# Optimization experiments

Measured on AMD Instinct MI355X. Metric: run time of the kernel, lower is better.

## Reference

```python
import jax, jax.numpy as jnp
import numpy as np

T, B, D_IN, D_HID, D_OUT = 2048, 64, 256, 256, 256


def setup_inputs() -> dict:
    key = jax.random.key(0)
    k1, k2, k3, k4 = jax.random.split(key, 4)
    s_in = 1.0 / np.sqrt(D_IN)
    s_h = 1.0 / np.sqrt(D_HID)
    return {
        "x": jax.random.normal(k1, (T, B, D_IN), dtype=jnp.float32),
        "h": jnp.zeros((B, D_HID), dtype=jnp.float32),
        "W_in": jax.random.uniform(k2, (D_HID, D_IN), jnp.float32, -s_in, s_in),
        "W_hid": jax.random.uniform(k3, (D_HID, D_HID), jnp.float32, -s_h, s_h),
        "W_out": jax.random.uniform(k4, (D_OUT, D_HID), jnp.float32, -s_h, s_h),
    }


def reference(x, h, W_in, W_hid, W_out):
    # Precompute input projections for all timesteps in one big matmul: [T,B,H]
    x_proj = jnp.einsum("tbi,hi->tbh", x, W_in)

    def step(h_prev, xp_t):
        h_new = jnp.tanh(xp_t + h_prev @ W_hid.T)
        return h_new, h_new

    h_last, hs = jax.lax.scan(step, h, x_proj)  # hs: [T,B,H]
    ys = jnp.einsum("tbh,oh->tbo", hs, W_out).reshape(-1, W_out.shape[0])
    return ys, h_last
```

## Files before the change

kernel.cpp:

```cpp
#include <hip/hip_runtime.h>
#include <hip/hip_bf16.h>

#define TSTEPS 2048
#define NB 64
#define DH 256
#define NBDH (NB * DH)

typedef __attribute__((ext_vector_type(8))) short short8;
typedef __attribute__((ext_vector_type(4))) float f32x4;
typedef __attribute__((ext_vector_type(4))) int i32x4;

#define WSCALE 2032.0f
#define HSCALE 127.0f
#define INVSC (1.0f / (2032.0f * 127.0f))

__device__ __forceinline__ unsigned short f2bf(float f) {
  union { float f; unsigned u; } v; v.f = f;
  unsigned u = v.u;
  u += 0x7FFFu + ((u >> 16) & 1u);
  return (unsigned short)(u >> 16);
}

__device__ __forceinline__ float fast_tanh(float x) {
  float e = __builtin_amdgcn_exp2f(x * 2.885390081777927f);
  return 1.0f - 2.0f * __builtin_amdgcn_rcpf(e + 1.0f);
}

__device__ __forceinline__ int p2c(int p) {
  int q = p & 31;
  return (p & ~31) | ((q & 1) << 4) | (q >> 1);
}

__global__ void cvt_w(const float* __restrict__ win, const float* __restrict__ whid,
                      const float* __restrict__ wout, unsigned short* __restrict__ wbf,
                      char* __restrict__ wq) {
  int i = blockIdx.x * 256 + threadIdx.x;
  int mat = i >> 16, idx = i & 65535;
  int n = idx >> 8, klin = idx & 255;
  if (mat == 0) {
    wbf[idx] = f2bf(win[idx]);
  } else {
    const float* m = (mat == 1) ? whid : wout;
    float v = m[n * 256 + p2c(klin)] * WSCALE;
    int q = (int)__builtin_rintf(fminf(fmaxf(v, -127.f), 127.f));
    wq[(mat - 1) * 65536 + idx] = (char)q;
  }
}

__global__ __launch_bounds__(256) void gemm_in(
    const float* __restrict__ x, const unsigned short* __restrict__ Wbf,
    float* __restrict__ Cout) {
  const int w = threadIdx.x >> 6, l = threadIdx.x & 63;
  const int m16 = l & 15, kg = l >> 4;
  const long tile0 = ((long)blockIdx.x * 4 + w) * 2;

  short8 afr[2][8];
  for (int ti = 0; ti < 2; ++ti) {
    const float* ar = x + ((tile0 + ti) * 16 + m16) * 256 + kg * 8;
    for (int ks = 0; ks < 8; ++ks) {
      float4 f0 = *(const float4*)(ar + ks * 32);
      float4 f1 = *(const float4*)(ar + ks * 32 + 4);
      short8 s;
      s[0] = (short)f2bf(f0.x); s[1] = (short)f2bf(f0.y);
      s[2] = (short)f2bf(f0.z); s[3] = (short)f2bf(f0.w);
      s[4] = (short)f2bf(f1.x); s[5] = (short)f2bf(f1.y);
      s[6] = (short)f2bf(f1.z); s[7] = (short)f2bf(f1.w);
      afr[ti][ks] = s;
    }
  }
  for (int nt = 0; nt < 16; ++nt) {
    const int n = nt * 16 + m16;
    const unsigned short* wr = Wbf + n * 256 + kg * 8;
    f32x4 acc0 = {0.f, 0.f, 0.f, 0.f}, acc1 = {0.f, 0.f, 0.f, 0.f};
    for (int ks = 0; ks < 8; ++ks) {
      short8 b = *(const short8*)(wr + ks * 32);
      acc0 = __builtin_amdgcn_mfma_f32_16x16x32_bf16(afr[0][ks], b, acc0, 0, 0, 0);
      acc1 = __builtin_amdgcn_mfma_f32_16x16x32_bf16(afr[1][ks], b, acc1, 0, 0, 0);
    }
    for (int r = 0; r < 4; ++r) {
      Cout[(tile0 * 16 + kg * 4 + r) * 256 + n]       = acc0[r];
      Cout[((tile0 + 1) * 16 + kg * 4 + r) * 256 + n] = acc1[r];
    }
  }
}

__global__ __launch_bounds__(512, 2) void rnn_scan(
    const float* __restrict__ xp, const char* __restrict__ Wq,
    const float* __restrict__ h0, float* __restrict__ ys,
    float* __restrict__ hlast) {
  __shared__ __align__(16) char hq[2][256];
  const int tid = threadIdx.x, w = tid >> 6, l = tid & 63;
  const int b = blockIdx.x;
  const int m16 = l & 15, kg = l >> 4;

  i32x4 bq[2][4], by[2][4];
  for (int nt = 0; nt < 2; ++nt) {
    const char* wr = Wq + (w * 32 + nt * 16 + m16) * 256 + kg * 16;
    for (int ks = 0; ks < 4; ++ks) {
      bq[nt][ks] = *(const i32x4*)(wr + ks * 64);
      by[nt][ks] = *(const i32x4*)(wr + 65536 + ks * 64);
    }
  }

  if (tid < 256) {
    float v = fminf(fmaxf(h0[b * 256 + p2c(tid)], -1.f), 1.f) * HSCALE;
    hq[0][tid] = (char)(int)__builtin_rintf(v);
  }
  __syncthreads();

  const char* rda = &hq[0][0] + kg * 16;
  const float* xpb = xp + (long)b * 256 + w * 32 + m16;
  float* ysb = ys + (long)b * 256 + w * 32 + l;

  float xv0[2], xv1[2], xv2[2], xv3[2];
  if (l < 16) {
    xv0[0] = xpb[0];               xv0[1] = xpb[16];
    xv1[0] = xpb[1L * NBDH];       xv1[1] = xpb[1L * NBDH + 16];
    xv2[0] = xpb[2L * NBDH];       xv2[1] = xpb[2L * NBDH + 16];
    xv3[0] = xpb[3L * NBDH];       xv3[1] = xpb[3L * NBDH + 16];
  }

#define MI8(A, B, C) __builtin_amdgcn_mfma_i32_16x16x64_i8(A, B, C, 0, 0, 0)
#define RNN_STEP(T, CUR, XV, PF)                                              \
  {                                                                           \
    const char* ap = rda + (CUR) * 256;                                       \
    i32x4 a0 = *(const i32x4*)(ap);                                           \
    i32x4 a1 = *(const i32x4*)(ap + 64);                                      \
    i32x4 a2 = *(const i32x4*)(ap + 128);                                     \
    i32x4 a3 = *(const i32x4*)(ap + 192);                                     \
    float xq0 = XV[0], xq1 = XV[1];         \
    i32x4 c0 = {0, 0, 0, 0}, c1 = {0, 0, 0, 0};                               \
    if ((PF) && l < 16) {               \
      const float* q = xpb + (long)((T) + 4) * NBDH;                          \
      XV[0] = q[0]; XV[1] = q[16];                                            \
    }                                                                         \
    c0 = MI8(a0, bq[0][0], c0); c1 = MI8(a0, bq[1][0], c1);                   \
    c0 = MI8(a1, bq[0][1], c0); c1 = MI8(a1, bq[1][1], c1);                   \
    c0 = MI8(a2, bq[0][2], c0); c1 = MI8(a2, bq[1][2], c1);                   \
    c0 = MI8(a3, bq[0][3], c0); c1 = MI8(a3, bq[1][3], c1);                   \
    i32x4 y0 = {0, 0, 0, 0}, y1 = {0, 0, 0, 0};   \
    y0 = MI8(a0, by[0][0], y0); y1 = MI8(a0, by[1][0], y1);                   \
    y0 = MI8(a1, by[0][1], y0); y1 = MI8(a1, by[1][1], y1);                   \
    y0 = MI8(a2, by[0][2], y0); y1 = MI8(a2, by[1][2], y1);                   \
    y0 = MI8(a3, by[0][3], y0); y1 = MI8(a3, by[1][3], y1);                   \
    float z0 = (float)c0[0] * INVSC + xq0;                                    \
    float z1 = (float)c1[0] * INVSC + xq1;                                    \
    float t0 = fast_tanh(z0), t1 = fast_tanh(z1);                             \
    int q0 = (int)__builtin_rintf(t0 * HSCALE);                               \
    int q1 = (int)__builtin_rintf(t1 * HSCALE);                               \
    unsigned short uq = (unsigned short)((q0 & 0xFF) | ((q1 & 0xFF) << 8));   \
    if (l < 16) {                                                             \
      *(unsigned short*)(&hq[(CUR) ^ 1][w * 32 + 2 * l]) = uq;                \
      if ((T) > 0) {                                                          \
        ysb[(long)((T) - 1) * NBDH]      = (float)y0[0] * INVSC;              \
        ysb[(long)((T) - 1) * NBDH + 16] = (float)y1[0] * INVSC;              \
      }                                                                       \
      if ((T) == TSTEPS - 1) {                                                \
        hlast[b * 256 + w * 32 + l]      = t0;                                \
        hlast[b * 256 + w * 32 + 16 + l] = t1;                                \
      }                                                                       \
    }                                                                         \
    asm volatile("s_waitcnt lgkmcnt(0)" ::: "memory");    \
    __builtin_amdgcn_s_barrier();                                             \
    __builtin_amdgcn_sched_barrier(0);                                        \
  }

#pragma unroll 1
  for (int t = 0; t < TSTEPS - 4; t += 4) {
    RNN_STEP(t, 0, xv0, true);
    RNN_STEP(t + 1, 1, xv1, true);
    RNN_STEP(t + 2, 0, xv2, true);
    RNN_STEP(t + 3, 1, xv3, true);
  }
  RNN_STEP(TSTEPS - 4, 0, xv0, false);
  RNN_STEP(TSTEPS - 3, 1, xv1, false);
  RNN_STEP(TSTEPS - 2, 0, xv2, false);
  RNN_STEP(TSTEPS - 1, 1, xv3, false);
#undef RNN_STEP

  {
    const char* ap = rda;
    i32x4 a0 = *(const i32x4*)(ap);
    i32x4 a1 = *(const i32x4*)(ap + 64);
    i32x4 a2 = *(const i32x4*)(ap + 128);
    i32x4 a3 = *(const i32x4*)(ap + 192);
    i32x4 y0 = {0, 0, 0, 0}, y1 = {0, 0, 0, 0};
    y0 = MI8(a0, by[0][0], y0); y1 = MI8(a0, by[1][0], y1);
    y0 = MI8(a1, by[0][1], y0); y1 = MI8(a1, by[1][1], y1);
    y0 = MI8(a2, by[0][2], y0); y1 = MI8(a2, by[1][2], y1);
    y0 = MI8(a3, by[0][3], y0); y1 = MI8(a3, by[1][3], y1);
    if (l < 16) {
      ysb[(long)(TSTEPS - 1) * NBDH]      = (float)y0[0] * INVSC;
      ysb[(long)(TSTEPS - 1) * NBDH + 16] = (float)y1[0] * INVSC;
    }
  }
#undef MI8
}

extern "C" void kernel_launch(void* const* d_in, const int* in_sizes, int n_in,
                              void* d_out, int out_size, void* d_ws, size_t ws_size,
                              hipStream_t stream) {
  const float* x    = (const float*)d_in[0];
  const float* h0   = (const float*)d_in[1];
  const float* Win  = (const float*)d_in[2];
  const float* Whid = (const float*)d_in[3];
  const float* Wout = (const float*)d_in[4];
  float* ys    = (float*)d_out;
  float* hlast = ys + (long)TSTEPS * NB * 256;

  unsigned short* wbf_in = (unsigned short*)d_ws;
  char* wq = (char*)d_ws + 131072;
  float* xproj = (float*)((char*)d_ws + 262144);

  cvt_w<<<dim3(768), dim3(256), 0, stream>>>(Win, Whid, Wout, wbf_in, wq);
  gemm_in<<<dim3(1024), dim3(256), 0, stream>>>(x, wbf_in, xproj);
  rnn_scan<<<dim3(64), dim3(512), 0, stream>>>(xproj, wq, h0, ys, hlast);
}
```

Before: 954.9 us.

## Split recurrence and output projection across separate waves; store input projection as packed bf16

```diff
diff --git a/kernel.cpp b/kernel.cpp
--- a/kernel.cpp
+++ b/kernel.cpp
@@ -49,7 +49,7 @@
 
 __global__ __launch_bounds__(256) void gemm_in(
     const float* __restrict__ x, const unsigned short* __restrict__ Wbf,
-    float* __restrict__ Cout) {
+    unsigned* __restrict__ xpk) {
   const int w = threadIdx.x >> 6, l = threadIdx.x & 63;
   const int m16 = l & 15, kg = l >> 4;
   const long tile0 = ((long)blockIdx.x * 4 + w) * 2;
@@ -68,37 +68,50 @@
       afr[ti][ks] = s;
     }
   }
-  for (int nt = 0; nt < 16; ++nt) {
-    const int n = nt * 16 + m16;
-    const unsigned short* wr = Wbf + n * 256 + kg * 8;
-    f32x4 acc0 = {0.f, 0.f, 0.f, 0.f}, acc1 = {0.f, 0.f, 0.f, 0.f};
+  for (int g = 0; g < 8; ++g) {
+    const unsigned short* wr0 = Wbf + (g * 32 + m16) * 256 + kg * 8;
+    const unsigned short* wr1 = Wbf + (g * 32 + 16 + m16) * 256 + kg * 8;
+    f32x4 a00 = {0,0,0,0}, a01 = {0,0,0,0}, a10 = {0,0,0,0}, a11 = {0,0,0,0};
     for (int ks = 0; ks < 8; ++ks) {
-      short8 b = *(const short8*)(wr + ks * 32);
-      acc0 = __builtin_amdgcn_mfma_f32_16x16x32_bf16(afr[0][ks], b, acc0, 0, 0, 0);
-      acc1 = __builtin_amdgcn_mfma_f32_16x16x32_bf16(afr[1][ks], b, acc1, 0, 0, 0);
+      short8 b0 = *(const short8*)(wr0 + ks * 32);
+      short8 b1 = *(const short8*)(wr1 + ks * 32);
+      a00 = __builtin_amdgcn_mfma_f32_16x16x32_bf16(afr[0][ks], b0, a00, 0, 0, 0);
+      a10 = __builtin_amdgcn_mfma_f32_16x16x32_bf16(afr[1][ks], b0, a10, 0, 0, 0);
+      a01 = __builtin_amdgcn_mfma_f32_16x16x32_bf16(afr[0][ks], b1, a01, 0, 0, 0);
+      a11 = __builtin_amdgcn_mfma_f32_16x16x32_bf16(afr[1][ks], b1, a11, 0, 0, 0);
     }
     for (int r = 0; r < 4; ++r) {
-      Cout[(tile0 * 16 + kg * 4 + r) * 256 + n]       = acc0[r];
-      Cout[((tile0 + 1) * 16 + kg * 4 + r) * 256 + n] = acc1[r];
-    }
-  }
-}
-
-__global__ __launch_bounds__(512, 2) void rnn_scan(
-    const float* __restrict__ xp, const char* __restrict__ Wq,
+      unsigned p0, p1;
+      asm("v_cvt_pk_bf16_f32 %0, %1, %2" : "=v"(p0) : "v"(a00[r]), "v"(a01[r]));
+      asm("v_cvt_pk_bf16_f32 %0, %1, %2" : "=v"(p1) : "v"(a10[r]), "v"(a11[r]));
+      xpk[(tile0 * 16 + kg * 4 + r) * 128 + g * 16 + m16]       = p0;
+      xpk[((tile0 + 1) * 16 + kg * 4 + r) * 128 + g * 16 + m16] = p1;
+    }
+  }
+}
+
+__global__ __launch_bounds__(768, 1) void rnn_scan(
+    const unsigned* __restrict__ xpk, const char* __restrict__ Wq,
     const float* __restrict__ h0, float* __restrict__ ys,
     float* __restrict__ hlast) {
   __shared__ __align__(16) char hq[2][256];
-  const int tid = threadIdx.x, w = tid >> 6, l = tid & 63;
+  const int tid = threadIdx.x, wid = tid >> 6, l = tid & 63;
   const int b = blockIdx.x;
   const int m16 = l & 15, kg = l >> 4;
-
-  i32x4 bq[2][4], by[2][4];
-  for (int nt = 0; nt < 2; ++nt) {
-    const char* wr = Wq + (w * 32 + nt * 16 + m16) * 256 + kg * 16;
-    for (int ks = 0; ks < 4; ++ks) {
-      bq[nt][ks] = *(const i32x4*)(wr + ks * 64);
-      by[nt][ks] = *(const i32x4*)(wr + 65536 + ks * 64);
+  const bool isy = (wid >= 8);
+  const int w = isy ? (wid - 8) : wid;
+
+  i32x4 bq[2][4];
+  i32x4 by[4][4];
+  if (!isy) {
+    for (int nt = 0; nt < 2; ++nt) {
+      const char* wr = Wq + (w * 32 + nt * 16 + m16) * 256 + kg * 16;
+      for (int ks = 0; ks < 4; ++ks) bq[nt][ks] = *(const i32x4*)(wr + ks * 64);
+    }
+  } else {
+    for (int nt = 0; nt < 4; ++nt) {
+      const char* wr = Wq + 65536 + (w * 64 + nt * 16 + m16) * 256 + kg * 16;
+      for (int ks = 0; ks < 4; ++ks) by[nt][ks] = *(const i32x4*)(wr + ks * 64);
     }
   }
 
@@ -109,15 +122,15 @@
   __syncthreads();
 
   const char* rda = &hq[0][0] + kg * 16;
-  const float* xpb = xp + (long)b * 256 + w * 32 + m16;
-  float* ysb = ys + (long)b * 256 + w * 32 + l;
-
-  float xv0[2], xv1[2], xv2[2], xv3[2];
-  if (l < 16) {
-    xv0[0] = xpb[0];               xv0[1] = xpb[16];
-    xv1[0] = xpb[1L * NBDH];       xv1[1] = xpb[1L * NBDH + 16];
-    xv2[0] = xpb[2L * NBDH];       xv2[1] = xpb[2L * NBDH + 16];
-    xv3[0] = xpb[3L * NBDH];       xv3[1] = xpb[3L * NBDH + 16];
+  const unsigned* xpb = xpk + (long)b * 128 + w * 16 + l;
+  float* ysb = ys + (long)b * 256 + w * 64 + l;
+
+  unsigned xv0 = 0, xv1 = 0, xv2 = 0, xv3 = 0;
+  if (!isy && l < 16) {
+    xv0 = xpb[0];
+    xv1 = xpb[1L * 8192];
+    xv2 = xpb[2L * 8192];
+    xv3 = xpb[3L * 8192];
   }
 
 #define MI8(A, B, C) __builtin_amdgcn_mfma_i32_16x16x64_i8(A, B, C, 0, 0, 0)
@@ -128,36 +141,45 @@
     i32x4 a1 = *(const i32x4*)(ap + 64);                                      \
     i32x4 a2 = *(const i32x4*)(ap + 128);                                     \
     i32x4 a3 = *(const i32x4*)(ap + 192);                                     \
-    float xq0 = XV[0], xq1 = XV[1];         \
-    i32x4 c0 = {0, 0, 0, 0}, c1 = {0, 0, 0, 0};                               \
-    if ((PF) && l < 16) {               \
-      const float* q = xpb + (long)((T) + 4) * NBDH;                          \
-      XV[0] = q[0]; XV[1] = q[16];                                            \
-    }                                                                         \
-    c0 = MI8(a0, bq[0][0], c0); c1 = MI8(a0, bq[1][0], c1);                   \
-    c0 = MI8(a1, bq[0][1], c0); c1 = MI8(a1, bq[1][1], c1);                   \
-    c0 = MI8(a2, bq[0][2], c0); c1 = MI8(a2, bq[1][2], c1);                   \
-    c0 = MI8(a3, bq[0][3], c0); c1 = MI8(a3, bq[1][3], c1);                   \
-    i32x4 y0 = {0, 0, 0, 0}, y1 = {0, 0, 0, 0};   \
-    y0 = MI8(a0, by[0][0], y0); y1 = MI8(a0, by[1][0], y1);                   \
-    y0 = MI8(a1, by[0][1], y0); y1 = MI8(a1, by[1][1], y1);                   \
-    y0 = MI8(a2, by[0][2], y0); y1 = MI8(a2, by[1][2], y1);                   \
-    y0 = MI8(a3, by[0][3], y0); y1 = MI8(a3, by[1][3], y1);                   \
-    float z0 = (float)c0[0] * INVSC + xq0;                                    \
-    float z1 = (float)c1[0] * INVSC + xq1;                                    \
-    float t0 = fast_tanh(z0), t1 = fast_tanh(z1);                             \
-    int q0 = (int)__builtin_rintf(t0 * HSCALE);                               \
-    int q1 = (int)__builtin_rintf(t1 * HSCALE);                               \
-    unsigned short uq = (unsigned short)((q0 & 0xFF) | ((q1 & 0xFF) << 8));   \
-    if (l < 16) {                                                             \
-      *(unsigned short*)(&hq[(CUR) ^ 1][w * 32 + 2 * l]) = uq;                \
-      if ((T) > 0) {                                                          \
-        ysb[(long)((T) - 1) * NBDH]      = (float)y0[0] * INVSC;              \
-        ysb[(long)((T) - 1) * NBDH + 16] = (float)y1[0] * INVSC;              \
+    if (!isy) {                                                               \
+      unsigned xc = XV;                     \
+      if ((PF) && l < 16) XV = xpb[(long)((T) + 4) * 8192];                   \
+      i32x4 c0 = {0, 0, 0, 0}, c1 = {0, 0, 0, 0};                             \
+      c0 = MI8(a0, bq[0][0], c0); c1 = MI8(a0, bq[1][0], c1);                 \
+      c0 = MI8(a1, bq[0][1], c0); c1 = MI8(a1, bq[1][1], c1);                 \
+      c0 = MI8(a2, bq[0][2], c0); c1 = MI8(a2, bq[1][2], c1);                 \
+      c0 = MI8(a3, bq[0][3], c0); c1 = MI8(a3, bq[1][3], c1);                 \
+      union { unsigned u; float f; } u0, u1;                                  \
+      u0.u = xc << 16; u1.u = xc & 0xffff0000u;                               \
+      float z0 = (float)c0[0] * INVSC + u0.f;                                 \
+      float z1 = (float)c1[0] * INVSC + u1.f;                                 \
+      float t0 = fast_tanh(z0), t1 = fast_tanh(z1);                           \
+      int q0 = (int)__builtin_rintf(t0 * HSCALE);                             \
+      int q1 = (int)__builtin_rintf(t1 * HSCALE);                             \
+      unsigned short uq = (unsigned short)((q0 & 0xFF) | ((q1 & 0xFF) << 8)); \
+      if (l < 16) {                                                           \
+        *(unsigned short*)(&hq[(CUR) ^ 1][w * 32 + 2 * l]) = uq;              \
+        if ((T) == TSTEPS - 1) {                                              \
+          hlast[b * 256 + w * 32 + l]      = t0;                              \
+          hlast[b * 256 + w * 32 + 16 + l] = t1;                              \
+        }                                                                     \
       }                                                                       \
-      if ((T) == TSTEPS - 1) {                                                \
-        hlast[b * 256 + w * 32 + l]      = t0;                                \
-        hlast[b * 256 + w * 32 + 16 + l] = t1;                                \
+    } else {                                                                  \
+      i32x4 y0 = {0,0,0,0}, y1 = {0,0,0,0}, y2 = {0,0,0,0}, y3 = {0,0,0,0};   \
+      y0 = MI8(a0, by[0][0], y0); y1 = MI8(a0, by[1][0], y1);                 \
+      y2 = MI8(a0, by[2][0], y2); y3 = MI8(a0, by[3][0], y3);                 \
+      y0 = MI8(a1, by[0][1], y0); y1 = MI8(a1, by[1][1], y1);                 \
+      y2 = MI8(a1, by[2][1], y2); y3 = MI8(a1, by[3][1], y3);                 \
+      y0 = MI8(a2, by[0][2], y0); y1 = MI8(a2, by[1][2], y1);                 \
+      y2 = MI8(a2, by[2][2], y2); y3 = MI8(a2, by[3][2], y3);                 \
+      y0 = MI8(a3, by[0][3], y0); y1 = MI8(a3, by[1][3], y1);                 \
+      y2 = MI8(a3, by[2][3], y2); y3 = MI8(a3, by[3][3], y3);                 \
+      if ((T) > 0 && l < 16) {                    \
+        float* yr = ysb + (long)((T) - 1) * NBDH;                             \
+        yr[0]  = (float)y0[0] * INVSC;                                        \
+        yr[16] = (float)y1[0] * INVSC;                                        \
+        yr[32] = (float)y2[0] * INVSC;                                        \
+        yr[48] = (float)y3[0] * INVSC;                                        \
       }                                                                       \
     }                                                                         \
     asm volatile("s_waitcnt lgkmcnt(0)" ::: "memory");    \
@@ -178,20 +200,27 @@
   RNN_STEP(TSTEPS - 1, 1, xv3, false);
 #undef RNN_STEP
 
-  {
+  if (isy) {
     const char* ap = rda;
     i32x4 a0 = *(const i32x4*)(ap);
     i32x4 a1 = *(const i32x4*)(ap + 64);
     i32x4 a2 = *(const i32x4*)(ap + 128);
     i32x4 a3 = *(const i32x4*)(ap + 192);
-    i32x4 y0 = {0, 0, 0, 0}, y1 = {0, 0, 0, 0};
+    i32x4 y0 = {0,0,0,0}, y1 = {0,0,0,0}, y2 = {0,0,0,0}, y3 = {0,0,0,0};
     y0 = MI8(a0, by[0][0], y0); y1 = MI8(a0, by[1][0], y1);
+    y2 = MI8(a0, by[2][0], y2); y3 = MI8(a0, by[3][0], y3);
     y0 = MI8(a1, by[0][1], y0); y1 = MI8(a1, by[1][1], y1);
+    y2 = MI8(a1, by[2][1], y2); y3 = MI8(a1, by[3][1], y3);
     y0 = MI8(a2, by[0][2], y0); y1 = MI8(a2, by[1][2], y1);
+    y2 = MI8(a2, by[2][2], y2); y3 = MI8(a2, by[3][2], y3);
     y0 = MI8(a3, by[0][3], y0); y1 = MI8(a3, by[1][3], y1);
+    y2 = MI8(a3, by[2][3], y2); y3 = MI8(a3, by[3][3], y3);
     if (l < 16) {
-      ysb[(long)(TSTEPS - 1) * NBDH]      = (float)y0[0] * INVSC;
-      ysb[(long)(TSTEPS - 1) * NBDH + 16] = (float)y1[0] * INVSC;
+      float* yr = ysb + (long)(TSTEPS - 1) * NBDH;
+      yr[0]  = (float)y0[0] * INVSC;
+      yr[16] = (float)y1[0] * INVSC;
+      yr[32] = (float)y2[0] * INVSC;
+      yr[48] = (float)y3[0] * INVSC;
     }
   }
 #undef MI8
@@ -210,9 +239,9 @@
 
   unsigned short* wbf_in = (unsigned short*)d_ws;
   char* wq = (char*)d_ws + 131072;
-  float* xproj = (float*)((char*)d_ws + 262144);
+  unsigned* xpk = (unsigned*)((char*)d_ws + 262144);
 
   cvt_w<<<dim3(768), dim3(256), 0, stream>>>(Win, Whid, Wout, wbf_in, wq);
-  gemm_in<<<dim3(1024), dim3(256), 0, stream>>>(x, wbf_in, xproj);
-  rnn_scan<<<dim3(64), dim3(512), 0, stream>>>(xproj, wq, h0, ys, hlast);
-}
+  gemm_in<<<dim3(1024), dim3(256), 0, stream>>>(x, wbf_in, xpk);
+  rnn_scan<<<dim3(64), dim3(768), 0, stream>>>(xpk, wq, h0, ys, hlast);
+}
```

New measurement: 1.010 ms. 1.06x slower.

## Move output projection out of serial scan into separate int8 GEMM; store xproj as bf16

Applied to the files above, without the earlier changes.

```diff
diff --git a/kernel.cpp b/kernel.cpp
--- a/kernel.cpp
+++ b/kernel.cpp
@@ -49,7 +49,7 @@
 
 __global__ __launch_bounds__(256) void gemm_in(
     const float* __restrict__ x, const unsigned short* __restrict__ Wbf,
-    float* __restrict__ Cout) {
+    unsigned* __restrict__ xpk) {
   const int w = threadIdx.x >> 6, l = threadIdx.x & 63;
   const int m16 = l & 15, kg = l >> 4;
   const long tile0 = ((long)blockIdx.x * 4 + w) * 2;
@@ -68,38 +68,41 @@
       afr[ti][ks] = s;
     }
   }
-  for (int nt = 0; nt < 16; ++nt) {
-    const int n = nt * 16 + m16;
-    const unsigned short* wr = Wbf + n * 256 + kg * 8;
-    f32x4 acc0 = {0.f, 0.f, 0.f, 0.f}, acc1 = {0.f, 0.f, 0.f, 0.f};
+  for (int g = 0; g < 8; ++g) {
+    const unsigned short* wr0 = Wbf + (g * 32 + m16) * 256 + kg * 8;
+    const unsigned short* wr1 = Wbf + (g * 32 + 16 + m16) * 256 + kg * 8;
+    f32x4 a00 = {0,0,0,0}, a01 = {0,0,0,0}, a10 = {0,0,0,0}, a11 = {0,0,0,0};
     for (int ks = 0; ks < 8; ++ks) {
-      short8 b = *(const short8*)(wr + ks * 32);
-      acc0 = __builtin_amdgcn_mfma_f32_16x16x32_bf16(afr[0][ks], b, acc0, 0, 0, 0);
-      acc1 = __builtin_amdgcn_mfma_f32_16x16x32_bf16(afr[1][ks], b, acc1, 0, 0, 0);
+      short8 b0 = *(const short8*)(wr0 + ks * 32);
+      short8 b1 = *(const short8*)(wr1 + ks * 32);
+      a00 = __builtin_amdgcn_mfma_f32_16x16x32_bf16(afr[0][ks], b0, a00, 0, 0, 0);
+      a10 = __builtin_amdgcn_mfma_f32_16x16x32_bf16(afr[1][ks], b0, a10, 0, 0, 0);
+      a01 = __builtin_amdgcn_mfma_f32_16x16x32_bf16(afr[0][ks], b1, a01, 0, 0, 0);
+      a11 = __builtin_amdgcn_mfma_f32_16x16x32_bf16(afr[1][ks], b1, a11, 0, 0, 0);
     }
     for (int r = 0; r < 4; ++r) {
-      Cout[(tile0 * 16 + kg * 4 + r) * 256 + n]       = acc0[r];
-      Cout[((tile0 + 1) * 16 + kg * 4 + r) * 256 + n] = acc1[r];
+      unsigned p0, p1;
+      asm("v_cvt_pk_bf16_f32 %0, %1, %2" : "=v"(p0) : "v"(a00[r]), "v"(a01[r]));
+      asm("v_cvt_pk_bf16_f32 %0, %1, %2" : "=v"(p1) : "v"(a10[r]), "v"(a11[r]));
+      xpk[(tile0 * 16 + kg * 4 + r) * 128 + g * 16 + m16]       = p0;
+      xpk[((tile0 + 1) * 16 + kg * 4 + r) * 128 + g * 16 + m16] = p1;
     }
   }
 }
 
 __global__ __launch_bounds__(512, 2) void rnn_scan(
-    const float* __restrict__ xp, const char* __restrict__ Wq,
-    const float* __restrict__ h0, float* __restrict__ ys,
+    const unsigned* __restrict__ xpk, const char* __restrict__ Wq,
+    const float* __restrict__ h0, char* __restrict__ hsq,
     float* __restrict__ hlast) {
   __shared__ __align__(16) char hq[2][256];
   const int tid = threadIdx.x, w = tid >> 6, l = tid & 63;
   const int b = blockIdx.x;
   const int m16 = l & 15, kg = l >> 4;
 
-  i32x4 bq[2][4], by[2][4];
+  i32x4 bq[2][4];
   for (int nt = 0; nt < 2; ++nt) {
     const char* wr = Wq + (w * 32 + nt * 16 + m16) * 256 + kg * 16;
-    for (int ks = 0; ks < 4; ++ks) {
-      bq[nt][ks] = *(const i32x4*)(wr + ks * 64);
-      by[nt][ks] = *(const i32x4*)(wr + 65536 + ks * 64);
-    }
+    for (int ks = 0; ks < 4; ++ks) bq[nt][ks] = *(const i32x4*)(wr + ks * 64);
   }
 
   if (tid < 256) {
@@ -109,15 +112,15 @@
   __syncthreads();
 
   const char* rda = &hq[0][0] + kg * 16;
-  const float* xpb = xp + (long)b * 256 + w * 32 + m16;
-  float* ysb = ys + (long)b * 256 + w * 32 + l;
-
-  float xv0[2], xv1[2], xv2[2], xv3[2];
+  const unsigned* xpb = xpk + (long)b * 128 + w * 16 + l;
+  char* hsb = hsq + (long)b * 256 + w * 32 + 2 * m16;
+
+  unsigned xv0 = 0, xv1 = 0, xv2 = 0, xv3 = 0;
   if (l < 16) {
-    xv0[0] = xpb[0];               xv0[1] = xpb[16];
-    xv1[0] = xpb[1L * NBDH];       xv1[1] = xpb[1L * NBDH + 16];
-    xv2[0] = xpb[2L * NBDH];       xv2[1] = xpb[2L * NBDH + 16];
-    xv3[0] = xpb[3L * NBDH];       xv3[1] = xpb[3L * NBDH + 16];
+    xv0 = xpb[0];
+    xv1 = xpb[1L * 8192];
+    xv2 = xpb[2L * 8192];
+    xv3 = xpb[3L * 8192];
   }
 
 #define MI8(A, B, C) __builtin_amdgcn_mfma_i32_16x16x64_i8(A, B, C, 0, 0, 0)
@@ -128,33 +131,24 @@
     i32x4 a1 = *(const i32x4*)(ap + 64);                                      \
     i32x4 a2 = *(const i32x4*)(ap + 128);                                     \
     i32x4 a3 = *(const i32x4*)(ap + 192);                                     \
-    float xq0 = XV[0], xq1 = XV[1];         \
+    unsigned xc = XV;                       \
     i32x4 c0 = {0, 0, 0, 0}, c1 = {0, 0, 0, 0};                               \
-    if ((PF) && l < 16) {               \
-      const float* q = xpb + (long)((T) + 4) * NBDH;                          \
-      XV[0] = q[0]; XV[1] = q[16];                                            \
-    }                                                                         \
+    if ((PF) && l < 16) XV = xpb[(long)((T) + 4) * 8192];                     \
     c0 = MI8(a0, bq[0][0], c0); c1 = MI8(a0, bq[1][0], c1);                   \
     c0 = MI8(a1, bq[0][1], c0); c1 = MI8(a1, bq[1][1], c1);                   \
     c0 = MI8(a2, bq[0][2], c0); c1 = MI8(a2, bq[1][2], c1);                   \
     c0 = MI8(a3, bq[0][3], c0); c1 = MI8(a3, bq[1][3], c1);                   \
-    i32x4 y0 = {0, 0, 0, 0}, y1 = {0, 0, 0, 0};   \
-    y0 = MI8(a0, by[0][0], y0); y1 = MI8(a0, by[1][0], y1);                   \
-    y0 = MI8(a1, by[0][1], y0); y1 = MI8(a1, by[1][1], y1);                   \
-    y0 = MI8(a2, by[0][2], y0); y1 = MI8(a2, by[1][2], y1);                   \
-    y0 = MI8(a3, by[0][3], y0); y1 = MI8(a3, by[1][3], y1);                   \
-    float z0 = (float)c0[0] * INVSC + xq0;                                    \
-    float z1 = (float)c1[0] * INVSC + xq1;                                    \
+    union { unsigned u; float f; } u0, u1;                                    \
+    u0.u = xc << 16; u1.u = xc & 0xffff0000u;                                 \
+    float z0 = (float)c0[0] * INVSC + u0.f;                                   \
+    float z1 = (float)c1[0] * INVSC + u1.f;                                   \
     float t0 = fast_tanh(z0), t1 = fast_tanh(z1);                             \
     int q0 = (int)__builtin_rintf(t0 * HSCALE);                               \
     int q1 = (int)__builtin_rintf(t1 * HSCALE);                               \
     unsigned short uq = (unsigned short)((q0 & 0xFF) | ((q1 & 0xFF) << 8));   \
     if (l < 16) {                                                             \
       *(unsigned short*)(&hq[(CUR) ^ 1][w * 32 + 2 * l]) = uq;                \
-      if ((T) > 0) {                                                          \
-        ysb[(long)((T) - 1) * NBDH]      = (float)y0[0] * INVSC;              \
-        ysb[(long)((T) - 1) * NBDH + 16] = (float)y1[0] * INVSC;              \
-      }                                                                       \
+      *(unsigned short*)(hsb + (long)(T) * NBDH) = uq;                        \
       if ((T) == TSTEPS - 1) {                                                \
         hlast[b * 256 + w * 32 + l]      = t0;                                \
         hlast[b * 256 + w * 32 + 16 + l] = t1;                                \
@@ -177,24 +171,35 @@
   RNN_STEP(TSTEPS - 2, 0, xv2, false);
   RNN_STEP(TSTEPS - 1, 1, xv3, false);
 #undef RNN_STEP
-
-  {
-    const char* ap = rda;
-    i32x4 a0 = *(const i32x4*)(ap);
-    i32x4 a1 = *(const i32x4*)(ap + 64);
-    i32x4 a2 = *(const i32x4*)(ap + 128);
-    i32x4 a3 = *(const i32x4*)(ap + 192);
-    i32x4 y0 = {0, 0, 0, 0}, y1 = {0, 0, 0, 0};
-    y0 = MI8(a0, by[0][0], y0); y1 = MI8(a0, by[1][0], y1);
-    y0 = MI8(a1, by[0][1], y0); y1 = MI8(a1, by[1][1], y1);
-    y0 = MI8(a2, by[0][2], y0); y1 = MI8(a2, by[1][2], y1);
-    y0 = MI8(a3, by[0][3], y0); y1 = MI8(a3, by[1][3], y1);
-    if (l < 16) {
-      ysb[(long)(TSTEPS - 1) * NBDH]      = (float)y0[0] * INVSC;
-      ysb[(long)(TSTEPS - 1) * NBDH + 16] = (float)y1[0] * INVSC;
-    }
-  }
 #undef MI8
+}
+
+__global__ __launch_bounds__(256) void gemm_out(
+    const char* __restrict__ Aq, const char* __restrict__ Wq,
+    float* __restrict__ Cout) {
+  const int w = threadIdx.x >> 6, l = threadIdx.x & 63;
+  const int m16 = l & 15, kg = l >> 4;
+  const long tile0 = ((long)blockIdx.x * 4 + w) * 2;
+
+  i32x4 afr[2][4];
+  for (int ti = 0; ti < 2; ++ti) {
+    const char* ar = Aq + ((tile0 + ti) * 16 + m16) * 256 + kg * 16;
+    for (int ks = 0; ks < 4; ++ks) afr[ti][ks] = *(const i32x4*)(ar + ks * 64);
+  }
+  for (int nt = 0; nt < 16; ++nt) {
+    const int n = nt * 16 + m16;
+    const char* wr = Wq + n * 256 + kg * 16;
+    i32x4 acc0 = {0, 0, 0, 0}, acc1 = {0, 0, 0, 0};
+    for (int ks = 0; ks < 4; ++ks) {
+      i32x4 bv = *(const i32x4*)(wr + ks * 64);
+      acc0 = __builtin_amdgcn_mfma_i32_16x16x64_i8(afr[0][ks], bv, acc0, 0, 0, 0);
+      acc1 = __builtin_amdgcn_mfma_i32_16x16x64_i8(afr[1][ks], bv, acc1, 0, 0, 0);
+    }
+    for (int r = 0; r < 4; ++r) {
+      Cout[(tile0 * 16 + kg * 4 + r) * 256 + n]       = (float)acc0[r] * INVSC;
+      Cout[((tile0 + 1) * 16 + kg * 4 + r) * 256 + n] = (float)acc1[r] * INVSC;
+    }
+  }
 }
 
 extern "C" void kernel_launch(void* const* d_in, const int* in_sizes, int n_in,
@@ -210,9 +215,12 @@
 
   unsigned short* wbf_in = (unsigned short*)d_ws;
   char* wq = (char*)d_ws + 131072;
-  float* xproj = (float*)((char*)d_ws + 262144);
+  char* wq_out = wq + 65536;
+  unsigned* xpk = (unsigned*)((char*)d_ws + 262144);
+  char* hsq = (char*)d_ws + 262144 + (size_t)67108864;
 
   cvt_w<<<dim3(768), dim3(256), 0, stream>>>(Win, Whid, Wout, wbf_in, wq);
-  gemm_in<<<dim3(1024), dim3(256), 0, stream>>>(x, wbf_in, xproj);
-  rnn_scan<<<dim3(64), dim3(512), 0, stream>>>(xproj, wq, h0, ys, hlast);
-}
+  gemm_in<<<dim3(1024), dim3(256), 0, stream>>>(x, wbf_in, xpk);
+  rnn_scan<<<dim3(64), dim3(512), 0, stream>>>(xpk, wq, h0, hsq, hlast);
+  gemm_out<<<dim3(1024), dim3(256), 0, stream>>>(hsq, wq_out, ys);
+}
```

After: 804.0 us, median of 2. 1.19x faster.
